# Kernel tuning notes

Measured on AMD Instinct MI355X. Metric: run time of the kernel, lower is better.

Reference implementation:

```python
import jax, jax.numpy as jnp
import numpy as np

N_STATE = 1024
N_HEAD = 16
HEAD_DIM = N_STATE // N_HEAD
SCALE = HEAD_DIM ** (-0.25)


def setup_inputs() -> dict:
    key = jax.random.key(0)
    ks = jax.random.split(key, 9)
    B, S, D = 32, 1500, N_STATE
    std = 1.0 / np.sqrt(D)
    return {
        "hidden_states": jax.random.normal(ks[0], (B, 1, D), dtype=jnp.float32),
        "encoder_output": jax.random.normal(ks[1], (B, S, D), dtype=jnp.float32),
        "Wq": jax.random.normal(ks[2], (D, D), dtype=jnp.float32) * std,
        "bq": jax.random.normal(ks[3], (D,), dtype=jnp.float32) * std,
        "Wk": jax.random.normal(ks[4], (D, D), dtype=jnp.float32) * std,
        "Wv": jax.random.normal(ks[5], (D, D), dtype=jnp.float32) * std,
        "bv": jax.random.normal(ks[6], (D,), dtype=jnp.float32) * std,
        "Wo": jax.random.normal(ks[7], (D, D), dtype=jnp.float32) * std,
        "bo": jax.random.normal(ks[8], (D,), dtype=jnp.float32) * std,
    }


def reference(hidden_states, encoder_output, Wq, bq, Wk, Wv, bv, Wo, bo):
    B = hidden_states.shape[0]
    S = encoder_output.shape[1]
    # projections (torch F.linear: x @ W.T + b)
    q = hidden_states @ Wq.T + bq                  # [B, 1, D]
    k_original = encoder_output @ Wk.T             # [B, S, D] (no bias)
    v_original = encoder_output @ Wv.T + bv        # [B, S, D]

    q = q.reshape(B, 1, N_HEAD, HEAD_DIM).transpose(0, 2, 1, 3)         # [B,H,1,hd]
    k = k_original.reshape(B, S, N_HEAD, HEAD_DIM).transpose(0, 2, 1, 3)  # [B,H,S,hd]
    v = v_original.reshape(B, S, N_HEAD, HEAD_DIM).transpose(0, 2, 1, 3)  # [B,H,S,hd]

    # pre-scaled q and k, scores in fp32 softmax then cast back
    attn_weights = jnp.einsum('bhqd,bhkd->bhqk', q * SCALE, k * SCALE)  # [B,H,1,S]
    attn_weights = jax.nn.softmax(attn_weights.astype(jnp.float32), axis=-1).astype(q.dtype)
    attn_output = jnp.einsum('bhqk,bhkd->bhqd', attn_weights, v)        # [B,H,1,hd]
    attn_output = attn_output.transpose(0, 2, 1, 3).reshape(B, 1, N_STATE)
    attn_output = attn_output @ Wo.T + bo
    return attn_output, k_original, v_original
```

## Files before the change

### kernel.cpp

```cpp
#include <hip/hip_runtime.h>
#include <cstdint>
#include <cstddef>

#define D_MODEL 1024
#define NH      16
#define HD      64
#define B_SZ    32
#define SEQ     1500
#define MROWS   (B_SZ * SEQ)
#define KD      1024
#define NCH     16
#define PSTR    68

typedef __attribute__((ext_vector_type(8))) short bf16x8;
typedef __attribute__((ext_vector_type(4))) float f32x4;
typedef unsigned short u16;

__device__ __forceinline__ u16 f2b(float f) {
  unsigned int x = __float_as_uint(f);
  x = (x + 0x7FFFu + ((x >> 16) & 1u)) >> 16;
  return (u16)x;
}

#define CAST_BLOCKS 3072
#define QPROJ_BLOCKS 64

__global__ __launch_bounds__(256) void cast_all_q(const float* __restrict__ enc,
                                                  const float* __restrict__ Wk,
                                                  const float* __restrict__ Wv,
                                                  const float* __restrict__ hs,
                                                  const float* __restrict__ Wq,
                                                  const float* __restrict__ bq,
                                                  u16* __restrict__ encb,
                                                  u16* __restrict__ wkvb,
                                                  float* __restrict__ qs) {
  const int tid = threadIdx.x;
  if (blockIdx.x < CAST_BLOCKS) {
    const int NA = MROWS * KD / 8;
    const int NW = KD * KD / 8;
    int stride = CAST_BLOCKS * 256;
    for (int i = blockIdx.x * 256 + tid; i < NA + 2 * NW; i += stride) {
      const float* s; u16* d;
      if (i < NA)            { s = enc + (size_t)i * 8;            d = encb + (size_t)i * 8; }
      else if (i < NA + NW)  { size_t j = i - NA;      s = Wk + j * 8; d = wkvb + j * 8; }
      else                   { size_t j = i - NA - NW; s = Wv + j * 8; d = wkvb + (size_t)NW * 8 + j * 8; }
      const float4* s4 = reinterpret_cast<const float4*>(s);
      float4 a = s4[0], b = s4[1];
      u16 u[8];
      u[0]=f2b(a.x); u[1]=f2b(a.y); u[2]=f2b(a.z); u[3]=f2b(a.w);
      u[4]=f2b(b.x); u[5]=f2b(b.y); u[6]=f2b(b.z); u[7]=f2b(b.w);
      *reinterpret_cast<uint4*>(d) = *reinterpret_cast<const uint4*>(u);
    }
  } else {
    const int qb = blockIdx.x - CAST_BLOCKS;
    const int n  = qb * 16 + (tid & 15);
    const int bb = tid >> 4;
    const float4* wp  = (const float4*)(Wq + (size_t)n * D_MODEL);
    const float4* x0p = (const float4*)(hs + (size_t)bb * D_MODEL);
    const float4* x1p = (const float4*)(hs + (size_t)(bb + 16) * D_MODEL);
    float a0 = 0.f, a1 = 0.f;
    #pragma unroll 8
    for (int i = 0; i < D_MODEL / 4; ++i) {
      float4 w = wp[i], x0 = x0p[i], x1 = x1p[i];
      a0 += w.x * x0.x + w.y * x0.y + w.z * x0.z + w.w * x0.w;
      a1 += w.x * x1.x + w.y * x1.y + w.z * x1.z + w.w * x1.w;
    }
    const float bqn = bq[n];
    qs[(size_t)bb * D_MODEL + n]        = (a0 + bqn) * 0.125f;
    qs[(size_t)(bb + 16) * D_MODEL + n] = (a1 + bqn) * 0.125f;
  }
}

#define GBM 128
#define GBN 256
#define GBK 32
#define GNT (KD / GBK)

__device__ __forceinline__ void stageA(const u16* __restrict__ Ag, u16* lbuf,
                                       long m0, int kt, int tid) {
  int c = tid;
  int r = c >> 2, cp = c & 3;
  int scp = cp ^ ((r >> 1) & 3);
  const u16* src = Ag + (m0 + r) * (long)KD + kt * GBK + scp * 8;
  __builtin_amdgcn_global_load_lds((const __attribute__((address_space(1))) void*)src,
      (__attribute__((address_space(3))) void*)(lbuf + (size_t)c * 8), 16, 0, 0);
}

__device__ __forceinline__ void stageB(const u16* __restrict__ Bg, u16* lbuf,
                                       int n0, int kt, int tid) {
  #pragma unroll
  for (int L = 0; L < 2; ++L) {
    int c = tid + L * 512;
    int r = c >> 2, cp = c & 3;
    int scp = cp ^ ((r >> 1) & 3);
    const u16* src = Bg + (size_t)(n0 + r) * KD + kt * GBK + scp * 8;
    __builtin_amdgcn_global_load_lds((const __attribute__((address_space(1))) void*)src,
        (__attribute__((address_space(3))) void*)(lbuf + (size_t)c * 8), 16, 0, 0);
  }
}

__device__ __forceinline__ bf16x8 ldFrag(const u16* buf, int row, int lane) {
  int r  = row + (lane & 15);
  int ch = (lane >> 4) ^ ((r >> 1) & 3);
  return *(const bf16x8*)(buf + (size_t)r * GBK + ch * 8);
}

__global__ __launch_bounds__(512, 4) void gemm_kv(const u16* __restrict__ A,
                                                  const u16* __restrict__ Bm,
                                                  const float* __restrict__ bv,
                                                  float* __restrict__ Kout,
                                                  float* __restrict__ Vout) {
  __shared__ __align__(16) char smem[2 * (GBM + GBN) * GBK * 2];
  u16* sA0 = (u16*)smem;
  u16* sA1 = sA0 + GBM * GBK;
  u16* sB0 = sA1 + GBM * GBK;
  u16* sB1 = sB0 + GBN * GBK;

  const int tid  = threadIdx.x;
  const int lane = tid & 63;
  const int wid  = tid >> 6;
  const int wr   = wid >> 2;
  const int wc   = wid & 3;

  int bx = (blockIdx.x & 7) * (gridDim.x >> 3) + (blockIdx.x >> 3);
  const int  mt = bx >> 3;
  const int  nt = bx & 7;
  const long m0 = (long)mt * GBM;
  const int  n0 = nt * GBN;

  stageA(A, sA0, m0, 0, tid);
  stageB(Bm, sB0, n0, 0, tid);
  stageA(A, sA1, m0, 1, tid);
  stageB(Bm, sB1, n0, 1, tid);

  f32x4 acc[4][4] = {};

  for (int t = 0; t < GNT; ++t) {
    if (t == GNT - 1) { asm volatile("s_waitcnt vmcnt(0)" ::: "memory"); }
    else              { asm volatile("s_waitcnt vmcnt(3)" ::: "memory"); }
    __builtin_amdgcn_s_barrier();

    const u16* cA = (t & 1) ? sA1 : sA0;
    const u16* cB = (t & 1) ? sB1 : sB0;
    bf16x8 af[4], bfr[4];
    #pragma unroll
    for (int mf = 0; mf < 4; ++mf) af[mf]  = ldFrag(cA, wr * 64 + mf * 16, lane);
    #pragma unroll
    for (int nf = 0; nf < 4; ++nf) bfr[nf] = ldFrag(cB, wc * 64 + nf * 16, lane);
    asm volatile("s_waitcnt lgkmcnt(0)" ::: "memory");
    __builtin_amdgcn_s_barrier();

    if (t + 2 < GNT) {
      u16* pA = (t & 1) ? sA1 : sA0;
      u16* pB = (t & 1) ? sB1 : sB0;
      stageA(A, pA, m0, t + 2, tid);
      stageB(Bm, pB, n0, t + 2, tid);
    }

    #pragma unroll
    for (int mf = 0; mf < 4; ++mf)
      #pragma unroll
      for (int nf = 0; nf < 4; ++nf)
        acc[mf][nf] = __builtin_amdgcn_mfma_f32_16x16x32_bf16(af[mf], bfr[nf], acc[mf][nf], 0, 0, 0);
  }

  __syncthreads();
  float (*ep)[260] = (float(*)[260])smem;

  const bool isV = (nt >= 4);
  float* Co = isV ? Vout : Kout;
  const int ncol0 = isV ? (n0 - 1024) : n0;
  float4 bias4[4];
  #pragma unroll
  for (int k = 0; k < 4; ++k) {
    int c4 = (tid + 512 * k) & 63;
    bias4[k] = isV ? reinterpret_cast<const float4*>(bv)[(ncol0 >> 2) + c4]
                   : make_float4(0.f, 0.f, 0.f, 0.f);
  }

  #pragma unroll
  for (int p = 0; p < 4; ++p) {
    if (wr == (p >> 1)) {
      const int mfb = (p & 1) * 2;
      #pragma unroll
      for (int mm = 0; mm < 2; ++mm)
        #pragma unroll
        for (int nf = 0; nf < 4; ++nf)
          #pragma unroll
          for (int r = 0; r < 4; ++r)
            ep[mm * 16 + (lane >> 4) * 4 + r][wc * 64 + nf * 16 + (lane & 15)] =
                acc[mfb + mm][nf][r];
    }
    __syncthreads();
    #pragma unroll
    for (int k = 0; k < 4; ++k) {
      int idx = tid + 512 * k;
      int row = idx >> 6;
      int c4  = idx & 63;
      long grow = m0 + p * 32 + row;
      float4 v = *reinterpret_cast<const float4*>(&ep[row][c4 * 4]);
      v.x += bias4[k].x; v.y += bias4[k].y; v.z += bias4[k].z; v.w += bias4[k].w;
      *reinterpret_cast<float4*>(&Co[grow * D_MODEL + ncol0 + c4 * 4]) = v;
    }
    __syncthreads();
  }
}

__global__ __launch_bounds__(256) void attn_part(const float* __restrict__ qs,
                                                 const float* __restrict__ K,
                                                 const float* __restrict__ V,
                                                 float* __restrict__ part) {
  const int b = blockIdx.x >> 4;
  const int c = blockIdx.x & 15;
  const int tid = threadIdx.x;
  const int h = tid >> 4;
  const int j = tid & 15;
  const int s0 = (c * SEQ) >> 4;
  const int s1 = (((c + 1) * SEQ) >> 4);

  const float4 q4 = ((const float4*)(qs + (size_t)b * D_MODEL))[tid];
  float m = -1e30f, l = 0.f;
  float4 pv = make_float4(0.f, 0.f, 0.f, 0.f);

  int i = s0;
  for (; i + 2 <= s1; i += 2) {
    const float4 kA = ((const float4*)(K + (size_t)(b * SEQ + i) * D_MODEL))[tid];
    const float4 vA = ((const float4*)(V + (size_t)(b * SEQ + i) * D_MODEL))[tid];
    const float4 kB = ((const float4*)(K + (size_t)(b * SEQ + i + 1) * D_MODEL))[tid];
    const float4 vB = ((const float4*)(V + (size_t)(b * SEQ + i + 1) * D_MODEL))[tid];

    float sA = kA.x * q4.x + kA.y * q4.y + kA.z * q4.z + kA.w * q4.w;
    sA += __shfl_xor(sA, 1); sA += __shfl_xor(sA, 2);
    sA += __shfl_xor(sA, 4); sA += __shfl_xor(sA, 8);
    float mn = fmaxf(m, sA);
    float sc = __expf(m - mn);
    float p  = __expf(sA - mn);
    m = mn;
    l = l * sc + p;
    pv.x = pv.x * sc + p * vA.x; pv.y = pv.y * sc + p * vA.y;
    pv.z = pv.z * sc + p * vA.z; pv.w = pv.w * sc + p * vA.w;

    float sB = kB.x * q4.x + kB.y * q4.y + kB.z * q4.z + kB.w * q4.w;
    sB += __shfl_xor(sB, 1); sB += __shfl_xor(sB, 2);
    sB += __shfl_xor(sB, 4); sB += __shfl_xor(sB, 8);
    mn = fmaxf(m, sB);
    sc = __expf(m - mn);
    p  = __expf(sB - mn);
    m = mn;
    l = l * sc + p;
    pv.x = pv.x * sc + p * vB.x; pv.y = pv.y * sc + p * vB.y;
    pv.z = pv.z * sc + p * vB.z; pv.w = pv.w * sc + p * vB.w;
  }
  if (i < s1) {
    const float4 kA = ((const float4*)(K + (size_t)(b * SEQ + i) * D_MODEL))[tid];
    const float4 vA = ((const float4*)(V + (size_t)(b * SEQ + i) * D_MODEL))[tid];
    float sA = kA.x * q4.x + kA.y * q4.y + kA.z * q4.z + kA.w * q4.w;
    sA += __shfl_xor(sA, 1); sA += __shfl_xor(sA, 2);
    sA += __shfl_xor(sA, 4); sA += __shfl_xor(sA, 8);
    float mn = fmaxf(m, sA);
    float sc = __expf(m - mn);
    float p  = __expf(sA - mn);
    m = mn;
    l = l * sc + p;
    pv.x = pv.x * sc + p * vA.x; pv.y = pv.y * sc + p * vA.y;
    pv.z = pv.z * sc + p * vA.z; pv.w = pv.w * sc + p * vA.w;
  }

  float* pp = part + ((size_t)(b * NH + h) * NCH + c) * PSTR;
  *(float4*)(pp + j * 4) = pv;
  if (j == 0) { pp[64] = m; pp[65] = l; }
}

__global__ __launch_bounds__(256) void oproj_comb(const float* __restrict__ part,
                                                  const float* __restrict__ Wo,
                                                  const float* __restrict__ bo,
                                                  float* __restrict__ out) {
  const int b = blockIdx.x >> 3, ch = blockIdx.x & 7;
  const int tid = threadIdx.x;
  __shared__ float xs[D_MODEL];

  {
    const int h = tid >> 4;
    const int d = (tid & 15) * 4;
    const float* pp = part + (size_t)(b * NH + h) * NCH * PSTR;
    float M = -1e30f;
    #pragma unroll
    for (int cc = 0; cc < NCH; ++cc) M = fmaxf(M, pp[cc * PSTR + 64]);
    float Lsum = 0.f;
    float4 o = make_float4(0.f, 0.f, 0.f, 0.f);
    #pragma unroll
    for (int cc = 0; cc < NCH; ++cc) {
      const float wgt = __expf(pp[cc * PSTR + 64] - M);
      Lsum += pp[cc * PSTR + 65] * wgt;
      float4 pv = *(const float4*)(pp + cc * PSTR + d);
      o.x += pv.x * wgt; o.y += pv.y * wgt; o.z += pv.z * wgt; o.w += pv.w * wgt;
    }
    const float inv = 1.0f / Lsum;
    xs[h * HD + d]     = o.x * inv;
    xs[h * HD + d + 1] = o.y * inv;
    xs[h * HD + d + 2] = o.z * inv;
    xs[h * HD + d + 3] = o.w * inv;
  }
  __syncthreads();

  const int n = ch * 128 + (tid >> 1);
  const int half = tid & 1;
  const float4* wp = (const float4*)(Wo + (size_t)n * D_MODEL + half * 512);
  const float4* xp = (const float4*)xs + half * 128;
  float a = 0.f;
  #pragma unroll 8
  for (int i = 0; i < 128; ++i) {
    float4 w = wp[i], xv = xp[i];
    a += w.x * xv.x + w.y * xv.y + w.z * xv.z + w.w * xv.w;
  }
  a += __shfl_xor(a, 1);
  if (!half) out[(size_t)b * D_MODEL + n] = a + bo[n];
}

extern "C" void kernel_launch(void* const* d_in, const int* in_sizes, int n_in,
                              void* d_out, int out_size, void* d_ws, size_t ws_size,
                              hipStream_t stream) {
  const float* hs  = (const float*)d_in[0];
  const float* enc = (const float*)d_in[1];
  const float* Wq  = (const float*)d_in[2];
  const float* bq  = (const float*)d_in[3];
  const float* Wk  = (const float*)d_in[4];
  const float* Wv  = (const float*)d_in[5];
  const float* bv  = (const float*)d_in[6];
  const float* Wo  = (const float*)d_in[7];
  const float* bo  = (const float*)d_in[8];

  float* out   = (float*)d_out;
  float* attnO = out;
  float* Kout  = out + 32768;
  float* Vout  = Kout + (size_t)MROWS * D_MODEL;

  char* ws = (char*)d_ws;
  const size_t off_wkvb = (size_t)MROWS * D_MODEL * 2;
  const size_t off_qs   = off_wkvb + 4194304;
  const size_t off_part = off_qs + 131072;

  u16*   encb = (u16*)ws;
  u16*   wkvb = (u16*)(ws + off_wkvb);
  float* qs   = (float*)(ws + off_qs);
  float* part = (float*)(ws + off_part);

  cast_all_q<<<CAST_BLOCKS + QPROJ_BLOCKS, 256, 0, stream>>>(enc, Wk, Wv, hs, Wq, bq,
                                                             encb, wkvb, qs);

  gemm_kv<<<(MROWS / GBM) * (2048 / GBN), 512, 0, stream>>>(encb, wkvb, bv, Kout, Vout);

  attn_part<<<B_SZ * NCH, 256, 0, stream>>>(qs, Kout, Vout, part);
  oproj_comb<<<B_SZ * 8, 256, 0, stream>>>(part, Wo, bo, attnO);
}
```

Before: 453.6 us.

## Triple-buffer GEMM LDS pipeline and restructure bf16 cast kernel into unrolled partitions

```diff
diff --git a/kernel.cpp b/kernel.cpp
--- a/kernel.cpp
+++ b/kernel.cpp
@@ -22,7 +22,8 @@
   return (u16)x;
 }
 
-#define CAST_BLOCKS 3072
+#define ENC_BLOCKS 3000
+#define W_BLOCKS   64
 #define QPROJ_BLOCKS 64
 
 __global__ __launch_bounds__(256) void cast_all_q(const float* __restrict__ enc,
@@ -35,24 +36,32 @@
                                                   u16* __restrict__ wkvb,
                                                   float* __restrict__ qs) {
   const int tid = threadIdx.x;
-  if (blockIdx.x < CAST_BLOCKS) {
-    const int NA = MROWS * KD / 8;
-    const int NW = KD * KD / 8;
-    int stride = CAST_BLOCKS * 256;
-    for (int i = blockIdx.x * 256 + tid; i < NA + 2 * NW; i += stride) {
-      const float* s; u16* d;
-      if (i < NA)            { s = enc + (size_t)i * 8;            d = encb + (size_t)i * 8; }
-      else if (i < NA + NW)  { size_t j = i - NA;      s = Wk + j * 8; d = wkvb + j * 8; }
-      else                   { size_t j = i - NA - NW; s = Wv + j * 8; d = wkvb + (size_t)NW * 8 + j * 8; }
-      const float4* s4 = reinterpret_cast<const float4*>(s);
-      float4 a = s4[0], b = s4[1];
-      u16 u[8];
-      u[0]=f2b(a.x); u[1]=f2b(a.y); u[2]=f2b(a.z); u[3]=f2b(a.w);
-      u[4]=f2b(b.x); u[5]=f2b(b.y); u[6]=f2b(b.z); u[7]=f2b(b.w);
-      *reinterpret_cast<uint4*>(d) = *reinterpret_cast<const uint4*>(u);
+  const int bid = blockIdx.x;
+  if (bid < ENC_BLOCKS) {
+    const float4* s4 = (const float4*)enc;
+    const size_t base = (size_t)bid * 256 + tid;
+    #pragma unroll
+    for (int k = 0; k < 16; ++k) {
+      size_t i = base + (size_t)k * (ENC_BLOCKS * 256);
+      float4 a = s4[i];
+      u16 u[4] = { f2b(a.x), f2b(a.y), f2b(a.z), f2b(a.w) };
+      *reinterpret_cast<uint2*>(encb + i * 4) = *reinterpret_cast<const uint2*>(u);
+    }
+  } else if (bid < ENC_BLOCKS + W_BLOCKS) {
+    const int wb = bid - ENC_BLOCKS;
+    const size_t base = (size_t)wb * 256 + tid;
+    const int NW4 = KD * KD / 4;
+    #pragma unroll
+    for (int k = 0; k < 32; ++k) {
+      size_t i = base + (size_t)k * (W_BLOCKS * 256);
+      const float4* s4 = (i < (size_t)NW4) ? (const float4*)Wk : (const float4*)Wv;
+      size_t j = (i < (size_t)NW4) ? i : i - NW4;
+      float4 a = s4[j];
+      u16 u[4] = { f2b(a.x), f2b(a.y), f2b(a.z), f2b(a.w) };
+      *reinterpret_cast<uint2*>(wkvb + i * 4) = *reinterpret_cast<const uint2*>(u);
     }
   } else {
-    const int qb = blockIdx.x - CAST_BLOCKS;
+    const int qb = bid - ENC_BLOCKS - W_BLOCKS;
     const int n  = qb * 16 + (tid & 15);
     const int bb = tid >> 4;
     const float4* wp  = (const float4*)(Wq + (size_t)n * D_MODEL);
@@ -75,6 +84,8 @@
 #define GBN 256
 #define GBK 32
 #define GNT (KD / GBK)
+#define AT  (GBM * GBK)
+#define BT  (GBN * GBK)
 
 __device__ __forceinline__ void stageA(const u16* __restrict__ Ag, u16* lbuf,
                                        long m0, int kt, int tid) {
@@ -110,11 +121,9 @@
                                                   const float* __restrict__ bv,
                                                   float* __restrict__ Kout,
                                                   float* __restrict__ Vout) {
-  __shared__ __align__(16) char smem[2 * (GBM + GBN) * GBK * 2];
-  u16* sA0 = (u16*)smem;
-  u16* sA1 = sA0 + GBM * GBK;
-  u16* sB0 = sA1 + GBM * GBK;
-  u16* sB1 = sB0 + GBN * GBK;
+  __shared__ __align__(16) char smem[3 * (GBM + GBN) * GBK * 2];
+  u16* sAb = (u16*)smem;
+  u16* sBb = sAb + 3 * AT;
 
   const int tid  = threadIdx.x;
   const int lane = tid & 63;
@@ -128,20 +137,24 @@
   const long m0 = (long)mt * GBM;
   const int  n0 = nt * GBN;
 
-  stageA(A, sA0, m0, 0, tid);
-  stageB(Bm, sB0, n0, 0, tid);
-  stageA(A, sA1, m0, 1, tid);
-  stageB(Bm, sB1, n0, 1, tid);
+  stageA(A, sAb + 0 * AT, m0, 0, tid);
+  stageB(Bm, sBb + 0 * BT, n0, 0, tid);
+  stageA(A, sAb + 1 * AT, m0, 1, tid);
+  stageB(Bm, sBb + 1 * BT, n0, 1, tid);
+  stageA(A, sAb + 2 * AT, m0, 2, tid);
+  stageB(Bm, sBb + 2 * BT, n0, 2, tid);
 
   f32x4 acc[4][4] = {};
 
   for (int t = 0; t < GNT; ++t) {
-    if (t == GNT - 1) { asm volatile("s_waitcnt vmcnt(0)" ::: "memory"); }
-    else              { asm volatile("s_waitcnt vmcnt(3)" ::: "memory"); }
+    if (t < GNT - 2)       { asm volatile("s_waitcnt vmcnt(6)" ::: "memory"); }
+    else if (t == GNT - 2) { asm volatile("s_waitcnt vmcnt(3)" ::: "memory"); }
+    else                   { asm volatile("s_waitcnt vmcnt(0)" ::: "memory"); }
     __builtin_amdgcn_s_barrier();
 
-    const u16* cA = (t & 1) ? sA1 : sA0;
-    const u16* cB = (t & 1) ? sB1 : sB0;
+    const int  bi = t % 3;
+    const u16* cA = sAb + bi * AT;
+    const u16* cB = sBb + bi * BT;
     bf16x8 af[4], bfr[4];
     #pragma unroll
     for (int mf = 0; mf < 4; ++mf) af[mf]  = ldFrag(cA, wr * 64 + mf * 16, lane);
@@ -150,11 +163,9 @@
     asm volatile("s_waitcnt lgkmcnt(0)" ::: "memory");
     __builtin_amdgcn_s_barrier();
 
-    if (t + 2 < GNT) {
-      u16* pA = (t & 1) ? sA1 : sA0;
-      u16* pB = (t & 1) ? sB1 : sB0;
-      stageA(A, pA, m0, t + 2, tid);
-      stageB(Bm, pB, n0, t + 2, tid);
+    if (t + 3 < GNT) {
+      stageA(A, sAb + bi * AT, m0, t + 3, tid);
+      stageB(Bm, sBb + bi * BT, n0, t + 3, tid);
     }
 
     #pragma unroll
@@ -345,8 +356,8 @@
   float* qs   = (float*)(ws + off_qs);
   float* part = (float*)(ws + off_part);
 
-  cast_all_q<<<CAST_BLOCKS + QPROJ_BLOCKS, 256, 0, stream>>>(enc, Wk, Wv, hs, Wq, bq,
-                                                             encb, wkvb, qs);
+  cast_all_q<<<ENC_BLOCKS + W_BLOCKS + QPROJ_BLOCKS, 256, 0, stream>>>(enc, Wk, Wv, hs, Wq, bq,
+                                                                       encb, wkvb, qs);
 
   gemm_kv<<<(MROWS / GBM) * (2048 / GBN), 512, 0, stream>>>(encb, wkvb, bv, Kout, Vout);
 
```

Measured after the change: 440.4 us (median of 2 runs). 1.03x faster.
